# Kernel optimization log

Hardware: AMD Instinct MI355X
Metric: run time of the kernel (lower is better)

## Reference

```python
import jax, jax.numpy as jnp
import numpy as np

TOP_K = 6  # num_experts_per_tok


def _glu_mlp(x, wg, wu, wd):
    # DeepSeek MLP: down( silu(gate(x)) * up(x) )
    return (jax.nn.silu(x @ wg) * (x @ wu)) @ wd


def setup_inputs() -> dict:
    key = jax.random.key(0)
    ks = jax.random.split(key, 8)
    B, S, D, E, F, FS = 2, 2048, 1024, 8, 512, 1024
    sc = 0.02
    return {
        "hidden_states": jax.random.normal(ks[0], (B, S, D), jnp.float32),
        "router_w": jax.random.normal(ks[1], (D, E), jnp.float32) * sc,
        "w_gate": jax.random.normal(ks[2], (E, D, F), jnp.float32) * sc,
        "w_up": jax.random.normal(ks[3], (E, D, F), jnp.float32) * sc,
        "w_down": jax.random.normal(ks[4], (E, F, D), jnp.float32) * sc,
        "ws_gate": jax.random.normal(ks[5], (D, FS), jnp.float32) * sc,
        "ws_up": jax.random.normal(ks[6], (D, FS), jnp.float32) * sc,
        "ws_down": jax.random.normal(ks[7], (FS, D), jnp.float32) * sc,
    }


def reference(hidden_states, router_w, w_gate, w_up, w_down, ws_gate, ws_up, ws_down):
    B, S, D = hidden_states.shape
    x = hidden_states.reshape(-1, D)                       # [T, D] tokens
    # Gate: softmax router + top-k (DeepSeek gate, no renorm)
    scores = jax.nn.softmax(x @ router_w, axis=-1)         # [T, E]
    topk_w, topk_idx = jax.lax.top_k(scores, TOP_K)        # [T, K]
    # Expert SiLU-GLU MLPs evaluated for all experts (math-identical to the
    # argsort dispatch -> grouped GEMM -> scatter combine in moe_infer)
    g = jnp.einsum('td,edf->etf', x, w_gate)               # [E, T, F]
    u = jnp.einsum('td,edf->etf', x, w_up)                 # [E, T, F]
    f_all = jnp.einsum('etf,efd->ted', jax.nn.silu(g) * u, w_down)  # [T, E, D]
    # Combine: final[t] = sum_k topk_w[t,k] * expert_{topk_idx[t,k]}(x[t])
    picked = jnp.take_along_axis(f_all, topk_idx[:, :, None], axis=1)  # [T, K, D]
    y = jnp.sum(picked * topk_w[:, :, None], axis=1).reshape(B, S, D)
    # shared experts branch
    y = y + _glu_mlp(hidden_states, ws_gate, ws_up, ws_down)
    return y
```

## Files before the change

kernel.cpp:

```cpp
#include <hip/hip_runtime.h>

typedef __attribute__((ext_vector_type(8))) short bf16x8;
typedef __attribute__((ext_vector_type(8))) unsigned short ushort8;
typedef __attribute__((ext_vector_type(4))) float floatx4;

static __device__ __forceinline__ unsigned short f2b(float f) {
  union { float f; unsigned int i; } v; v.f = f;
  unsigned int x = v.i;
  return (unsigned short)((x + 0x7fffu + ((x >> 16) & 1u)) >> 16);
}

#define GLDS(gp, lp) \
  __builtin_amdgcn_global_load_lds( \
      (const __attribute__((address_space(1))) unsigned int*)(gp), \
      (__attribute__((address_space(3))) unsigned int*)(lp), 16, 0, 0)

static __device__ __forceinline__ void swizzle_mn(int lin, int Mb, int Nb,
                                                  int& m_idx, int& n_idx) {
  if ((Mb & 7) == 0) {
    int xcd = lin & 7;
    int idx = lin >> 3;
    int nstrips = Mb >> 3;
    m_idx = (idx % nstrips) * 8 + xcd;
    n_idx = idx / nstrips;
  } else {
    m_idx = lin % Mb;
    n_idx = lin / Mb;
  }
}

__global__ __launch_bounds__(256) void router_cvt(
    const float* __restrict__ X, const float* __restrict__ RW,
    float* __restrict__ cw, unsigned short* __restrict__ Xb) {
  const int tid = threadIdx.x;
  const int wid = tid >> 6, lane = tid & 63;
  const int t = blockIdx.x * 4 + wid;
  const float* xp = X + (size_t)t * 1024;
  unsigned short* xo = Xb + (size_t)t * 1024;
  float acc[8];
#pragma unroll
  for (int e = 0; e < 8; e++) acc[e] = 0.f;
#pragma unroll
  for (int i = 0; i < 4; i++) {
    const int d0 = i * 256 + lane * 4;
    float4 v = *(const float4*)(xp + d0);
    ushort4 o;
    o.x = f2b(v.x); o.y = f2b(v.y); o.z = f2b(v.z); o.w = f2b(v.w);
    *(ushort4*)(xo + d0) = o;
    const float xv[4] = {v.x, v.y, v.z, v.w};
#pragma unroll
    for (int j = 0; j < 4; j++) {
      const float* r = RW + (size_t)(d0 + j) * 8;
      float4 r0 = *(const float4*)r;
      float4 r1 = *(const float4*)(r + 4);
      acc[0] += xv[j] * r0.x; acc[1] += xv[j] * r0.y;
      acc[2] += xv[j] * r0.z; acc[3] += xv[j] * r0.w;
      acc[4] += xv[j] * r1.x; acc[5] += xv[j] * r1.y;
      acc[6] += xv[j] * r1.z; acc[7] += xv[j] * r1.w;
    }
  }
#pragma unroll
  for (int m = 1; m < 64; m <<= 1) {
#pragma unroll
    for (int e = 0; e < 8; e++) acc[e] += __shfl_xor(acc[e], m);
  }
  if (lane == 0) {
    float mx = acc[0];
#pragma unroll
    for (int e = 1; e < 8; e++) mx = fmaxf(mx, acc[e]);
    float prob[8], s = 0.f;
#pragma unroll
    for (int e = 0; e < 8; e++) { prob[e] = expf(acc[e] - mx); s += prob[e]; }
    float inv = 1.f / s;
#pragma unroll
    for (int e = 0; e < 8; e++) prob[e] *= inv;
    int m1 = 0;
#pragma unroll
    for (int e = 1; e < 8; e++) if (prob[e] < prob[m1]) m1 = e;
    int m2 = -1;
#pragma unroll
    for (int e = 0; e < 8; e++)
      if (e != m1 && (m2 < 0 || prob[e] < prob[m2])) m2 = e;
#pragma unroll
    for (int e = 0; e < 8; e++)
      cw[(size_t)t * 8 + e] = (e == m1 || e == m2) ? 0.f : prob[e];
  }
}

__global__ __launch_bounds__(256) void transpose_all(
    const float* __restrict__ wg, const float* __restrict__ wu,
    const float* __restrict__ wd, const float* __restrict__ wsg,
    const float* __restrict__ wsu, const float* __restrict__ wsd,
    unsigned short* __restrict__ wgT, unsigned short* __restrict__ wuT,
    unsigned short* __restrict__ wdT, unsigned short* __restrict__ wsgT,
    unsigned short* __restrict__ wsuT, unsigned short* __restrict__ wsdT) {
  __shared__ __align__(16) unsigned short T[64 * 64];
  const int z = blockIdx.z;
  const float* src; unsigned short* dst; int K, N;
  if (z < 8)       { src = wg  + (size_t)z * 1024 * 512;        dst = wgT + (size_t)z * 512 * 1024;        K = 1024; N = 512; }
  else if (z < 16) { src = wu  + (size_t)(z - 8) * 1024 * 512;  dst = wuT + (size_t)(z - 8) * 512 * 1024;  K = 1024; N = 512; }
  else if (z < 24) { src = wd  + (size_t)(z - 16) * 512 * 1024; dst = wdT + (size_t)(z - 16) * 1024 * 512; K = 512;  N = 1024; }
  else if (z == 24){ src = wsg; dst = wsgT; K = 1024; N = 1024; }
  else if (z == 25){ src = wsu; dst = wsuT; K = 1024; N = 1024; }
  else             { src = wsd; dst = wsdT; K = 1024; N = 1024; }
  const int bn = blockIdx.x * 64, bk = blockIdx.y * 64;
  if (bn >= N || bk >= K) return;
  const int tid = threadIdx.x;
  {
    const int r = tid >> 4;
    const int c = (tid & 15) * 4;
#pragma unroll
    for (int i = 0; i < 4; i++) {
      const int rr = r + i * 16;
      float4 v = *(const float4*)(src + (size_t)(bk + rr) * N + bn + c);
      ushort4 o;
      o.x = f2b(v.x); o.y = f2b(v.y); o.z = f2b(v.z); o.w = f2b(v.w);
      *(ushort4*)(&T[rr * 64 + (c ^ (rr & 56))]) = o;
    }
  }
  __syncthreads();
  {
    const int n_ = tid >> 3;
    const int k0 = (tid & 7) * 8;
#pragma unroll
    for (int p = 0; p < 2; p++) {
      const int n = n_ + p * 32;
      ushort8 o;
#pragma unroll
      for (int j = 0; j < 8; j++) o[j] = T[(k0 + j) * 64 + (n ^ k0)];
      *(ushort8*)(dst + (size_t)(bn + n) * K + bk + k0) = o;
    }
  }
}

#define VMCNT(N) asm volatile("s_waitcnt vmcnt(" #N ")" ::: "memory")
#define BARS() do { __builtin_amdgcn_s_barrier(); \
                    __builtin_amdgcn_sched_barrier(0); } while (0)

#define STG_I0(K, BS) do { \
  GLDS(a0 + (K),          sm + (BS) + wid * 512); \
  GLDS(a0 + (K) + 131072, sm + (BS) + 8192 + wid * 512); } while (0)
#define STG_I1(K, BS) do { \
  GLDS(bg0 + (K),        sm + (BS) + 16384 + wid * 1024); \
  GLDS(bg0 + (K) + 8192, sm + (BS) + 16384 + wid * 1024 + 512); } while (0)
#define STG_I2(K, BS) do { \
  GLDS(bu0 + (K),        sm + (BS) + 24576 + wid * 1024); \
  GLDS(bu0 + (K) + 8192, sm + (BS) + 24576 + wid * 1024 + 512); } while (0)
#define STG_I3(K, BS) do { \
  GLDS(a0 + (K) + 65536,  sm + (BS) + 4096 + wid * 512); \
  GLDS(a0 + (K) + 196608, sm + (BS) + 12288 + wid * 512); } while (0)

#define READ_A(DST, DB, H) do { _Pragma("unroll") \
  for (int mf = 0; mf < 4; ++mf) { \
    const int row_ = wm * 128 + (H) * 64 + mf * 16 + lr; \
    const int rb_ = (DB) + row_ * 64; const int rx_ = row_ & 7; \
    DST[mf][0] = *(const bf16x8*)(sm + rb_ + ((quad ^ rx_) << 3)); \
    DST[mf][1] = *(const bf16x8*)(sm + rb_ + (((4 + quad) ^ rx_) << 3)); \
  } } while (0)

#define READ_B(DST, DB, RG) do { _Pragma("unroll") \
  for (int nf = 0; nf < 2; ++nf) { \
    const int row_ = wn * 32 + nf * 16 + lr; \
    const int rb_ = (DB) + (RG) + row_ * 64; const int rx_ = row_ & 7; \
    DST[nf][0] = *(const bf16x8*)(sm + rb_ + ((quad ^ rx_) << 3)); \
    DST[nf][1] = *(const bf16x8*)(sm + rb_ + (((4 + quad) ^ rx_) << 3)); \
  } } while (0)

#define MM(ACC, AF, BF) do { \
  __builtin_amdgcn_s_setprio(1); \
  _Pragma("unroll") \
  for (int mf = 0; mf < 4; ++mf) { _Pragma("unroll") \
    for (int nf = 0; nf < 2; ++nf) { \
      ACC[mf][nf] = __builtin_amdgcn_mfma_f32_16x16x32_bf16( \
          AF[mf][0], BF[nf][0], ACC[mf][nf], 0, 0, 0); \
      ACC[mf][nf] = __builtin_amdgcn_mfma_f32_16x16x32_bf16( \
          AF[mf][1], BF[nf][1], ACC[mf][nf], 0, 0, 0); \
    } } \
  __builtin_amdgcn_s_setprio(0); } while (0)

__global__ __launch_bounds__(512, 2) void gemm_gu_fused(
    const unsigned short* __restrict__ X,
    const unsigned short* __restrict__ WgTe,
    const unsigned short* __restrict__ WgTs,
    const unsigned short* __restrict__ WuTe,
    const unsigned short* __restrict__ WuTs,
    unsigned short* __restrict__ H,
    const float* __restrict__ cw, int Mb) {
  __shared__ __align__(16) unsigned short sm[65536];
  const int tid = threadIdx.x;
  const int wid = tid >> 6, lane = tid & 63;
  const int lr = lane & 15, quad = lane >> 4;
  const int wm = wid >> 2, wn = wid & 3;

  int m_idx, n_idx;
  {
    const int lin = blockIdx.x;
    const int xcd = lin & 7;
    const int idx = lin >> 3;
    m_idx = idx / 5;
    n_idx = xcd * 5 + (idx - m_idx * 5);
  }
  const int m0 = m_idx * 256;
  const int n0 = n_idx * 128;

  const unsigned short *Bg, *Bu;
  int eidx = -1;
  if (n0 < 4096) {
    eidx = n0 >> 9;
    size_t off = ((size_t)eidx * 512 + (n0 & 511)) * 1024;
    Bg = WgTe + off; Bu = WuTe + off;
  } else {
    size_t off = (size_t)(n0 - 4096) * 1024;
    Bg = WgTs + off; Bu = WuTs + off;
  }

  const int grow8 = lane >> 3;
  const int gcol = ((lane & 7) ^ grow8) << 3;
  const unsigned short* a0 =
      X + (size_t)(m0 + wid * 8 + grow8) * 1024 + gcol;
  const unsigned short* bg0 =
      Bg + (size_t)(wid * 16 + grow8) * 1024 + gcol;
  const unsigned short* bu0 =
      Bu + (size_t)(wid * 16 + grow8) * 1024 + gcol;

  floatx4 gg[2][4][2], uu[2][4][2];
#pragma unroll
  for (int h = 0; h < 2; h++)
#pragma unroll
    for (int mf = 0; mf < 4; mf++)
#pragma unroll
      for (int nf = 0; nf < 2; nf++) {
        gg[h][mf][nf] = (floatx4)0.f;
        uu[h][mf][nf] = (floatx4)0.f;
      }

  bf16x8 fA0[4][2], fA1[4][2], fBg[2][2], fBu[2][2];

  STG_I0(0, 0); STG_I1(0, 0); STG_I2(0, 0); STG_I3(0, 0);

  for (int t = 0; t < 15; ++t) {
    const int db = (t & 1) << 15;
    const int nb = 32768 - db;
    const int kn = (t + 1) * 64;
    STG_I0(kn, nb);
    VMCNT(6); BARS();
    READ_A(fA0, db, 0);
    READ_B(fBg, db, 16384);
    MM(gg[0], fA0, fBg);
    STG_I1(kn, nb);
    VMCNT(6); BARS();
    READ_B(fBu, db, 24576);
    MM(uu[0], fA0, fBu);
    STG_I2(kn, nb);
    VMCNT(6); BARS();
    READ_A(fA1, db, 1);
    MM(gg[1], fA1, fBg);
    STG_I3(kn, nb);
    BARS();
    MM(uu[1], fA1, fBu);
  }
  {
    const int db = 32768;
    VMCNT(4); BARS();
    READ_A(fA0, db, 0);
    READ_B(fBg, db, 16384);
    MM(gg[0], fA0, fBg);
    VMCNT(2); BARS();
    READ_B(fBu, db, 24576);
    MM(uu[0], fA0, fBu);
    VMCNT(0); BARS();
    READ_A(fA1, db, 1);
    MM(gg[1], fA1, fBg);
    MM(uu[1], fA1, fBu);
  }

#pragma unroll
  for (int h = 0; h < 2; h++) {
#pragma unroll
    for (int mf = 0; mf < 4; mf++) {
#pragma unroll
      for (int nf = 0; nf < 2; nf++) {
#pragma unroll
        for (int r = 0; r < 4; r++) {
          int row = m0 + wm * 128 + h * 64 + mf * 16 + quad * 4 + r;
          int col = n0 + wn * 32 + nf * 16 + lr;
          float g = gg[h][mf][nf][r];
          float u = uu[h][mf][nf][r];
          float s = (eidx >= 0) ? cw[(size_t)row * 8 + eidx] : 1.0f;
          float silu = g / (1.0f + __expf(-g));
          H[(size_t)row * 5120 + col] = f2b(s * silu * u);
        }
      }
    }
  }
}

#define DN_STG(KN, SBUF) do { \
  GLDS(Ha + (size_t)(KN),          smD + (SBUF) + wid * 512); \
  GLDS(Ha + (size_t)(KN) + 327680, smD + (SBUF) + 4096 + wid * 512); \
  const unsigned short *b0p_, *b1p_; \
  if ((KN) < 4096) { \
    const unsigned short* be_ = WdTe + ((size_t)((KN) >> 9)) * (1024 * 512) + ((KN) & 511); \
    b0p_ = be_ + (size_t)bn0 * 512 + gcol; \
    b1p_ = be_ + (size_t)(bn0 + 64) * 512 + gcol; \
  } else { \
    b0p_ = WdTs + (size_t)bn0 * 1024 + ((KN) - 4096) + gcol; \
    b1p_ = WdTs + (size_t)(bn0 + 64) * 1024 + ((KN) - 4096) + gcol; \
  } \
  GLDS(b0p_, smD + (SBUF) + 8192 + wid * 512); \
  GLDS(b1p_, smD + (SBUF) + 12288 + wid * 512); } while (0)

#define DN_TILE(T, BUF, SBUF, DOSTG, VM) do { \
  VMCNT(VM); BARS(); \
  if (DOSTG) { DN_STG(((T) + 3) * 64, SBUF); } \
  bf16x8 af_[4][2], bf_[2][2]; \
  _Pragma("unroll") \
  for (int mt = 0; mt < 4; ++mt) { \
    const int row_ = wm * 64 + mt * 16 + lr; \
    const int rb_ = (BUF) + row_ * 64; const int rx_ = row_ & 7; \
    af_[mt][0] = *(const bf16x8*)(smD + rb_ + ((quad ^ rx_) << 3)); \
    af_[mt][1] = *(const bf16x8*)(smD + rb_ + (((4 + quad) ^ rx_) << 3)); \
  } \
  _Pragma("unroll") \
  for (int nt = 0; nt < 2; ++nt) { \
    const int row_ = wn * 32 + nt * 16 + lr; \
    const int rb_ = (BUF) + 8192 + row_ * 64; const int rx_ = row_ & 7; \
    bf_[nt][0] = *(const bf16x8*)(smD + rb_ + ((quad ^ rx_) << 3)); \
    bf_[nt][1] = *(const bf16x8*)(smD + rb_ + (((4 + quad) ^ rx_) << 3)); \
  } \
  __builtin_amdgcn_s_setprio(1); \
  _Pragma("unroll") \
  for (int kt = 0; kt < 2; ++kt) \
    _Pragma("unroll") \
    for (int mt = 0; mt < 4; ++mt) \
      _Pragma("unroll") \
      for (int nt = 0; nt < 2; ++nt) \
        acc[mt][nt] = __builtin_amdgcn_mfma_f32_16x16x32_bf16( \
            af_[mt][kt], bf_[nt][kt], acc[mt][nt], 0, 0, 0); \
  __builtin_amdgcn_s_setprio(0); } while (0)

__global__ __launch_bounds__(512, 2) void gemm_down(
    const unsigned short* __restrict__ H,
    const unsigned short* __restrict__ WdTe,
    const unsigned short* __restrict__ WdTs,
    float* __restrict__ Y, int Mb) {
  __shared__ __align__(16) unsigned short smD[65536];
  const int tid = threadIdx.x;
  const int wid = tid >> 6, lane = tid & 63;
  const int lr = lane & 15, quad = lane >> 4;
  const int wm = wid >> 2, wn = wid & 3;
  int m_idx, n_idx;
  swizzle_mn(blockIdx.x, Mb, 8, m_idx, n_idx);
  const int m0 = m_idx * 128;
  const int n0 = n_idx * 128;

  const int grow8 = lane >> 3;
  const int gcol = ((lane & 7) ^ grow8) << 3;
  const unsigned short* Ha = H + (size_t)(m0 + wid * 8 + grow8) * 5120 + gcol;
  const int bn0 = n0 + wid * 8 + grow8;

  floatx4 acc[4][2];
#pragma unroll
  for (int i = 0; i < 4; i++)
#pragma unroll
    for (int j = 0; j < 2; j++) acc[i][j] = (floatx4)0.f;

  DN_STG(0, 0);
  DN_STG(64, 16384);
  DN_STG(128, 32768);

  for (int t = 0; t < 76; t += 4) {
    DN_TILE(t,     0,     49152, true, 8);
    DN_TILE(t + 1, 16384, 0,     true, 8);
    DN_TILE(t + 2, 32768, 16384, true, 8);
    DN_TILE(t + 3, 49152, 32768, true, 8);
  }
  DN_TILE(76, 0,     49152, true,  8);
  DN_TILE(77, 16384, 0,     false, 8);
  DN_TILE(78, 32768, 0,     false, 4);
  DN_TILE(79, 49152, 0,     false, 0);

#pragma unroll
  for (int mt = 0; mt < 4; mt++)
#pragma unroll
    for (int nt = 0; nt < 2; nt++)
#pragma unroll
      for (int r = 0; r < 4; r++) {
        int row = m0 + wm * 64 + mt * 16 + quad * 4 + r;
        int col = n0 + wn * 32 + nt * 16 + lr;
        Y[(size_t)row * 1024 + col] = acc[mt][nt][r];
      }
}

extern "C" void kernel_launch(void* const* d_in, const int* in_sizes, int n_in,
                              void* d_out, int out_size, void* d_ws, size_t ws_size,
                              hipStream_t stream) {
  const float* hs  = (const float*)d_in[0];
  const float* rw  = (const float*)d_in[1];
  const float* wg  = (const float*)d_in[2];
  const float* wu  = (const float*)d_in[3];
  const float* wd  = (const float*)d_in[4];
  const float* wsg = (const float*)d_in[5];
  const float* wsu = (const float*)d_in[6];
  const float* wsd = (const float*)d_in[7];
  float* out = (float*)d_out;

  char* p = (char*)d_ws;
  float* cw = (float*)p;                    p += (size_t)4096 * 8 * 4;
  unsigned short* Xb   = (unsigned short*)p; p += (size_t)4096 * 1024 * 2;
  unsigned short* wgT  = (unsigned short*)p; p += (size_t)8 * 512 * 1024 * 2;
  unsigned short* wuT  = (unsigned short*)p; p += (size_t)8 * 512 * 1024 * 2;
  unsigned short* wsgT = (unsigned short*)p; p += (size_t)1024 * 1024 * 2;
  unsigned short* wsuT = (unsigned short*)p; p += (size_t)1024 * 1024 * 2;
  unsigned short* wdT  = (unsigned short*)p; p += (size_t)8 * 1024 * 512 * 2;
  unsigned short* wsdT = (unsigned short*)p; p += (size_t)1024 * 1024 * 2;
  unsigned short* GH   = (unsigned short*)p;
  const size_t base_bytes = (size_t)(p - (char*)d_ws);

  int chunks = 8;
  for (int c = 1; c <= 8; c *= 2) {
    size_t gh_bytes = ((size_t)4096 / c) * 5120 * 2;
    if (base_bytes + gh_bytes <= ws_size) { chunks = c; break; }
  }
  const int rows = 4096 / chunks;
  const int Mb = rows / 128;
  const int MbG = rows / 256;

  router_cvt<<<1024, 256, 0, stream>>>(hs, rw, cw, Xb);
  transpose_all<<<dim3(16, 16, 27), 256, 0, stream>>>(
      wg, wu, wd, wsg, wsu, wsd, wgT, wuT, wdT, wsgT, wsuT, wsdT);

  for (int c = 0; c < chunks; c++) {
    const unsigned short* Xc = Xb + (size_t)c * rows * 1024;
    const float* cwc = cw + (size_t)c * rows * 8;
    float* outc = out + (size_t)c * rows * 1024;
    gemm_gu_fused<<<MbG * 40, 512, 0, stream>>>(
        Xc, wgT, wsgT, wuT, wsuT, GH, cwc, MbG);
    gemm_down<<<Mb * 8, 512, 0, stream>>>(GH, wdT, wsdT, outc, Mb);
  }
}
```

Before: 297.5 us.

## Route tokens per expert and skip gate/up GEMM for unselected tokens

The router now builds per-expert token lists with atomics, and the gate/up GEMM gathers only routed token rows per expert instead of computing all 8 experts for every token. The H buffer is zeroed first so rows for unrouted experts contribute nothing in the down GEMM. This cuts the expert gate/up compute by roughly a quarter (6 of 8 experts active) at the cost of an extra zeroing kernel, atomics, and gathered A loads. It also drops the chunking fallback and assumes the workspace holds the full H buffer.

```diff
diff --git a/kernel.cpp b/kernel.cpp
--- a/kernel.cpp
+++ b/kernel.cpp
@@ -29,9 +29,30 @@
   }
 }
 
+__global__ void zero_hx(unsigned short* __restrict__ H,
+                        int* __restrict__ tokList, int* __restrict__ cnt) {
+  const int b = blockIdx.x;
+  if (b < 2048) {
+    const int tidg = b * 256 + threadIdx.x;
+#pragma unroll
+    for (int i = 0; i < 4; i++) {
+      const int c8 = tidg + i * 524288;
+      const int row = c8 >> 9;
+      const int col = (c8 & 511) << 3;
+      *(uint4*)(H + (size_t)row * 5120 + col) = make_uint4(0u, 0u, 0u, 0u);
+    }
+  } else {
+    const int tid = (b - 2048) * 256 + threadIdx.x;
+#pragma unroll
+    for (int i = 0; i < 4; i++) tokList[tid * 4 + i] = 0;
+    if (b == 2048 && threadIdx.x < 8) cnt[threadIdx.x] = 0;
+  }
+}
+
 __global__ __launch_bounds__(256) void router_cvt(
     const float* __restrict__ X, const float* __restrict__ RW,
-    float* __restrict__ cw, unsigned short* __restrict__ Xb) {
+    float* __restrict__ cw, unsigned short* __restrict__ Xb,
+    int* __restrict__ tokList, int* __restrict__ cnt) {
   const int tid = threadIdx.x;
   const int wid = tid >> 6, lane = tid & 63;
   const int t = blockIdx.x * 4 + wid;
@@ -82,8 +103,14 @@
     for (int e = 0; e < 8; e++)
       if (e != m1 && (m2 < 0 || prob[e] < prob[m2])) m2 = e;
 #pragma unroll
-    for (int e = 0; e < 8; e++)
-      cw[(size_t)t * 8 + e] = (e == m1 || e == m2) ? 0.f : prob[e];
+    for (int e = 0; e < 8; e++) {
+      const bool act = (e != m1 && e != m2);
+      cw[(size_t)t * 8 + e] = act ? prob[e] : 0.f;
+      if (act) {
+        int pos = atomicAdd(&cnt[e], 1);
+        tokList[e * 4096 + pos] = t;
+      }
+    }
   }
 }
 
@@ -138,8 +165,8 @@
                     __builtin_amdgcn_sched_barrier(0); } while (0)
 
 #define STG_I0(K, BS) do { \
-  GLDS(a0 + (K),          sm + (BS) + wid * 512); \
-  GLDS(a0 + (K) + 131072, sm + (BS) + 8192 + wid * 512); } while (0)
+  GLDS(pA0 + (K), sm + (BS) + wid * 512); \
+  GLDS(pA2 + (K), sm + (BS) + 8192 + wid * 512); } while (0)
 #define STG_I1(K, BS) do { \
   GLDS(bg0 + (K),        sm + (BS) + 16384 + wid * 1024); \
   GLDS(bg0 + (K) + 8192, sm + (BS) + 16384 + wid * 1024 + 512); } while (0)
@@ -147,8 +174,8 @@
   GLDS(bu0 + (K),        sm + (BS) + 24576 + wid * 1024); \
   GLDS(bu0 + (K) + 8192, sm + (BS) + 24576 + wid * 1024 + 512); } while (0)
 #define STG_I3(K, BS) do { \
-  GLDS(a0 + (K) + 65536,  sm + (BS) + 4096 + wid * 512); \
-  GLDS(a0 + (K) + 196608, sm + (BS) + 12288 + wid * 512); } while (0)
+  GLDS(pA1 + (K), sm + (BS) + 4096 + wid * 512); \
+  GLDS(pA3 + (K), sm + (BS) + 12288 + wid * 512); } while (0)
 
 #define READ_A(DST, DB, H) do { _Pragma("unroll") \
   for (int mf = 0; mf < 4; ++mf) { \
@@ -178,50 +205,57 @@
     } } \
   __builtin_amdgcn_s_setprio(0); } while (0)
 
-__global__ __launch_bounds__(512, 2) void gemm_gu_fused(
+__global__ __launch_bounds__(512, 2) void gemm_gu_moe(
     const unsigned short* __restrict__ X,
     const unsigned short* __restrict__ WgTe,
     const unsigned short* __restrict__ WgTs,
     const unsigned short* __restrict__ WuTe,
     const unsigned short* __restrict__ WuTs,
     unsigned short* __restrict__ H,
-    const float* __restrict__ cw, int Mb) {
+    const float* __restrict__ cw,
+    const int* __restrict__ tokList, const int* __restrict__ cnt) {
   __shared__ __align__(16) unsigned short sm[65536];
+  __shared__ int ltok[256];
   const int tid = threadIdx.x;
   const int wid = tid >> 6, lane = tid & 63;
   const int lr = lane & 15, quad = lane >> 4;
   const int wm = wid >> 2, wn = wid & 3;
 
-  int m_idx, n_idx;
-  {
-    const int lin = blockIdx.x;
-    const int xcd = lin & 7;
-    const int idx = lin >> 3;
-    m_idx = idx / 5;
-    n_idx = xcd * 5 + (idx - m_idx * 5);
-  }
-  const int m0 = m_idx * 256;
-  const int n0 = n_idx * 128;
-
+  const int bid = blockIdx.x;
   const unsigned short *Bg, *Bu;
-  int eidx = -1;
-  if (n0 < 4096) {
-    eidx = n0 >> 9;
-    size_t off = ((size_t)eidx * 512 + (n0 & 511)) * 1024;
+  int eidx, pan, cntL;
+  if (bid < 512) {
+    eidx = bid >> 6;
+    const int sub = bid & 63;
+    const int mb = sub >> 2;
+    pan = sub & 3;
+    const int ce = cnt[eidx];
+    if (mb * 256 >= ce) return;
+    cntL = min(256, ce - mb * 256);
+    if (tid < 256) ltok[tid] = tokList[eidx * 4096 + mb * 256 + tid];
+    const size_t off = ((size_t)eidx * 512 + pan * 128) * 1024;
     Bg = WgTe + off; Bu = WuTe + off;
   } else {
-    size_t off = (size_t)(n0 - 4096) * 1024;
+    const int sub = bid - 512;
+    const int mb = sub >> 3;
+    pan = sub & 7;
+    eidx = -1;
+    cntL = 256;
+    if (tid < 256) ltok[tid] = mb * 256 + tid;
+    const size_t off = (size_t)(pan * 128) * 1024;
     Bg = WgTs + off; Bu = WuTs + off;
   }
+  __syncthreads();
 
   const int grow8 = lane >> 3;
   const int gcol = ((lane & 7) ^ grow8) << 3;
-  const unsigned short* a0 =
-      X + (size_t)(m0 + wid * 8 + grow8) * 1024 + gcol;
-  const unsigned short* bg0 =
-      Bg + (size_t)(wid * 16 + grow8) * 1024 + gcol;
-  const unsigned short* bu0 =
-      Bu + (size_t)(wid * 16 + grow8) * 1024 + gcol;
+  const int ar = wid * 8 + grow8;
+  const unsigned short* pA0 = X + (size_t)ltok[ar]       * 1024 + gcol;
+  const unsigned short* pA1 = X + (size_t)ltok[ar + 64]  * 1024 + gcol;
+  const unsigned short* pA2 = X + (size_t)ltok[ar + 128] * 1024 + gcol;
+  const unsigned short* pA3 = X + (size_t)ltok[ar + 192] * 1024 + gcol;
+  const unsigned short* bg0 = Bg + (size_t)(wid * 16 + grow8) * 1024 + gcol;
+  const unsigned short* bu0 = Bu + (size_t)(wid * 16 + grow8) * 1024 + gcol;
 
   floatx4 gg[2][4][2], uu[2][4][2];
 #pragma unroll
@@ -274,6 +308,7 @@
     MM(uu[1], fA1, fBu);
   }
 
+  const int colbase = (eidx >= 0) ? (eidx * 512 + pan * 128) : (4096 + pan * 128);
 #pragma unroll
   for (int h = 0; h < 2; h++) {
 #pragma unroll
@@ -282,13 +317,16 @@
       for (int nf = 0; nf < 2; nf++) {
 #pragma unroll
         for (int r = 0; r < 4; r++) {
-          int row = m0 + wm * 128 + h * 64 + mf * 16 + quad * 4 + r;
-          int col = n0 + wn * 32 + nf * 16 + lr;
-          float g = gg[h][mf][nf][r];
-          float u = uu[h][mf][nf][r];
-          float s = (eidx >= 0) ? cw[(size_t)row * 8 + eidx] : 1.0f;
-          float silu = g / (1.0f + __expf(-g));
-          H[(size_t)row * 5120 + col] = f2b(s * silu * u);
+          const int rowl = wm * 128 + h * 64 + mf * 16 + quad * 4 + r;
+          if (rowl < cntL) {
+            const int tok = ltok[rowl];
+            const int col = colbase + wn * 32 + nf * 16 + lr;
+            float g = gg[h][mf][nf][r];
+            float u = uu[h][mf][nf][r];
+            float s = (eidx >= 0) ? cw[(size_t)tok * 8 + eidx] : 1.0f;
+            float silu = g / (1.0f + __expf(-g));
+            H[(size_t)tok * 5120 + col] = f2b(s * silu * u);
+          }
         }
       }
     }
@@ -407,6 +445,8 @@
 
   char* p = (char*)d_ws;
   float* cw = (float*)p;                    p += (size_t)4096 * 8 * 4;
+  int* tokList = (int*)p;                   p += (size_t)8 * 4096 * 4;
+  int* cnt = (int*)p;                       p += 256;
   unsigned short* Xb   = (unsigned short*)p; p += (size_t)4096 * 1024 * 2;
   unsigned short* wgT  = (unsigned short*)p; p += (size_t)8 * 512 * 1024 * 2;
   unsigned short* wuT  = (unsigned short*)p; p += (size_t)8 * 512 * 1024 * 2;
@@ -415,27 +455,13 @@
   unsigned short* wdT  = (unsigned short*)p; p += (size_t)8 * 1024 * 512 * 2;
   unsigned short* wsdT = (unsigned short*)p; p += (size_t)1024 * 1024 * 2;
   unsigned short* GH   = (unsigned short*)p;
-  const size_t base_bytes = (size_t)(p - (char*)d_ws);
-
-  int chunks = 8;
-  for (int c = 1; c <= 8; c *= 2) {
-    size_t gh_bytes = ((size_t)4096 / c) * 5120 * 2;
-    if (base_bytes + gh_bytes <= ws_size) { chunks = c; break; }
-  }
-  const int rows = 4096 / chunks;
-  const int Mb = rows / 128;
-  const int MbG = rows / 256;
-
-  router_cvt<<<1024, 256, 0, stream>>>(hs, rw, cw, Xb);
+
+  zero_hx<<<2080, 256, 0, stream>>>(GH, tokList, cnt);
+  router_cvt<<<1024, 256, 0, stream>>>(hs, rw, cw, Xb, tokList, cnt);
   transpose_all<<<dim3(16, 16, 27), 256, 0, stream>>>(
       wg, wu, wd, wsg, wsu, wsd, wgT, wuT, wdT, wsgT, wsuT, wsdT);
 
-  for (int c = 0; c < chunks; c++) {
-    const unsigned short* Xc = Xb + (size_t)c * rows * 1024;
-    const float* cwc = cw + (size_t)c * rows * 8;
-    float* outc = out + (size_t)c * rows * 1024;
-    gemm_gu_fused<<<MbG * 40, 512, 0, stream>>>(
-        Xc, wgT, wsgT, wuT, wsuT, GH, cwc, MbG);
-    gemm_down<<<Mb * 8, 512, 0, stream>>>(GH, wdT, wsdT, outc, Mb);
-  }
-}
+  gemm_gu_moe<<<640, 512, 0, stream>>>(
+      Xb, wgT, wsgT, wuT, wsuT, GH, cw, tokList, cnt);
+  gemm_down<<<32 * 8, 512, 0, stream>>>(GH, wdT, wsdT, out, 32);
+}
```

After: 585.5 us. +96.8%, slower.
